# Optimization experiments

Hardware: AMD Instinct MI355X
Metric: run time of the kernel (lower is better)

Reference implementation:

```python
import jax, jax.numpy as jnp
import numpy as np

D, H = 128, 8
N_NODE, N_SRC = 50000, 100000
E_NBR, E_INC = 800000, 200000


def _seg_softmax(scores, idx, n):
    # scores: [E, H]; segmented softmax over segments given by idx
    mx = jax.ops.segment_max(scores, idx, num_segments=n)
    ex = jnp.exp(scores - mx[idx])
    sm = jax.ops.segment_sum(ex, idx, num_segments=n)
    return ex / (sm[idx] + 1e-12)


def _ln(x, g, b):
    m = jnp.mean(x, -1, keepdims=True)
    v = jnp.mean((x - m) ** 2, -1, keepdims=True)
    return g * (x - m) / jnp.sqrt(v + 1e-5) + b


def setup_inputs() -> dict:
    key = jax.random.key(0)
    ks = jax.random.split(key, 24)
    s = 1.0 / np.sqrt(D)
    inp = {
        'X': jax.random.normal(ks[0], (N_NODE, D), jnp.float32),
        'X_src': jax.random.normal(ks[1], (N_SRC, D), jnp.float32),
        'W_qkv': jax.random.normal(ks[2], (D, 3 * D), jnp.float32) * s,
        'w_bias': jax.random.normal(ks[3], (D, H), jnp.float32) * s,
        'W_gate': jax.random.normal(ks[4], (D, D), jnp.float32) * s,
        'b_gate': jnp.zeros((D,), jnp.float32),
        'W_o': jax.random.normal(ks[5], (D, D), jnp.float32) * s,
        'W_q': jax.random.normal(ks[6], (D, D), jnp.float32) * s,
        'W_kv': jax.random.normal(ks[7], (D, 2 * D), jnp.float32) * s,
        'w_bias_tgt': jax.random.normal(ks[8], (D, H), jnp.float32) * s,
        'w_bias_src': jax.random.normal(ks[9], (D, H), jnp.float32) * s,
        'W_gate_tgt': jax.random.normal(ks[10], (D, D), jnp.float32) * s,
        'b_gate_tgt': jnp.zeros((D,), jnp.float32),
        'W_gate_src': jax.random.normal(ks[11], (D, D), jnp.float32) * s,
        'b_gate_src': jnp.zeros((D,), jnp.float32),
        'W_o2': jax.random.normal(ks[12], (D, D), jnp.float32) * s,
        'ln1_g': jnp.ones((D,), jnp.float32),
        'ln1_b': jnp.zeros((D,), jnp.float32),
        'ln2_g': jnp.ones((D,), jnp.float32),
        'ln2_b': jnp.zeros((D,), jnp.float32),
        'nbr_src': jax.random.randint(ks[13], (E_NBR,), 0, N_NODE),
        'nbr_dst': jax.random.randint(ks[14], (E_NBR,), 0, N_NODE),
        'inc_tgt': jax.random.randint(ks[15], (E_INC,), 0, N_NODE),
        'inc_src': jax.random.randint(ks[16], (E_INC,), 0, N_SRC),
    }
    return inp


def reference(X, X_src, W_qkv, w_bias, W_gate, b_gate, W_o, W_q, W_kv,
              w_bias_tgt, w_bias_src, W_gate_tgt, b_gate_tgt, W_gate_src,
              b_gate_src, W_o2, ln1_g, ln1_b, ln2_g, ln2_b,
              nbr_src, nbr_dst, inc_tgt, inc_src):
    N = X.shape[0]
    dk = D // H
    scale = 1.0 / np.sqrt(dk)

    # --- SparseNeighbourhoodSelfAttn on level-0 cells ---
    qkv = (X @ W_qkv).reshape(N, 3, H, dk)
    Q, K, V = qkv[:, 0], qkv[:, 1], qkv[:, 2]            # [N,H,dk]
    scores = jnp.sum(Q[nbr_src] * K[nbr_dst], -1) * scale + (X @ w_bias)[nbr_src]  # [E,H]
    attn = _seg_softmax(scores, nbr_src, N)
    out = jax.ops.segment_sum(attn[..., None] * V[nbr_dst], nbr_src, num_segments=N)  # [N,H,dk]
    gate = jax.nn.sigmoid(X @ W_gate + b_gate).reshape(N, H, dk)
    sa = (gate * out).reshape(N, D) @ W_o
    h = _ln(X + sa, ln1_g, ln1_b)

    # --- SparseTopologicalCrossAttn from level-1 cells ---
    Qc = (h @ W_q).reshape(N, H, dk)
    kv = (X_src @ W_kv).reshape(-1, 2, H, dk)
    Kc, Vc = kv[:, 0], kv[:, 1]
    sc = (jnp.sum(Qc[inc_tgt] * Kc[inc_src], -1) * scale
          + (h @ w_bias_tgt)[inc_tgt] + (X_src @ w_bias_src)[inc_src])  # [Ei,H]
    attn_c = _seg_softmax(sc, inc_tgt, N)
    g_src = jax.nn.sigmoid(X_src @ W_gate_src + b_gate_src).reshape(-1, H, dk)
    out_c = jax.ops.segment_sum(attn_c[..., None] * (g_src[inc_src] * Vc[inc_src]),
                                inc_tgt, num_segments=N)
    g_tgt = jax.nn.sigmoid(h @ W_gate_tgt + b_gate_tgt).reshape(N, H, dk)
    ca = (g_tgt * out_c).reshape(N, D) @ W_o2
    return _ln(h + ca, ln2_g, ln2_b)
```

## Files before the change

### kernel.cpp

```cpp
#include <hip/hip_runtime.h>
#include <stdint.h>

__device__ __forceinline__ float bf_lo(uint32_t w) { return __uint_as_float(w << 16); }
__device__ __forceinline__ float bf_hi(uint32_t w) { return __uint_as_float(w & 0xffff0000u); }
__device__ __forceinline__ float bfu(uint16_t u) { return __uint_as_float((uint32_t)u << 16); }
__device__ __forceinline__ uint16_t f2bf(float f) {
    uint32_t u = __float_as_uint(f);
    uint32_t r = ((u >> 16) & 1u) + 0x7fffu;
    return (uint16_t)((u + r) >> 16);
}
__device__ __forceinline__ uint32_t pk2bf(float a, float b) {
    return (uint32_t)f2bf(a) | ((uint32_t)f2bf(b) << 16);
}
__device__ __forceinline__ void gload_lds16(const void* g, void* l) {
    __builtin_amdgcn_global_load_lds(
        (const __attribute__((address_space(1))) void*)g,
        (__attribute__((address_space(3))) void*)l, 16, 0, 0);
}

typedef __attribute__((ext_vector_type(8))) short bf16x8;
typedef __attribute__((ext_vector_type(4))) float f32x4;

#define LOG2E 1.4426950408889634f
#define QSC2  (0.25f * LOG2E)

#define M_BF16 0
#define M_QS   1
#define M_SIG  2
#define M_KVIK 3
#define M_KVIV 4
#define M_GV   5
#define M_LN1  6
#define M_LN2  7
#define M_B8   8

struct GemmJob {
    const uint16_t* A; const uint16_t* WT; const float* bias;
    const uint16_t* aux; const void* resid;
    const float* lng; const float* lnb;
    void* out; int M; int mode;
};
struct GemmJobs { GemmJob j[6]; };

__global__ __launch_bounds__(256) void multi_gemm_k(GemmJobs jobs)
{
    __shared__ uint16_t As[128 * 128];
    __shared__ uint16_t Ws[128 * 128];
    const GemmJob jb = jobs.j[blockIdx.y];
    const int m0 = blockIdx.x * 128;
    if (m0 >= jb.M) return;
    const int tid = threadIdx.x;
    const int wid = tid >> 6;
    const int lane = tid & 63;
    const int M = jb.M;

    {
        const uint16_t* Ab = jb.A + (size_t)m0 * 128;
        const uint16_t* Wb = jb.WT;
#pragma unroll
        for (int it = 0; it < 8; ++it) {
            int idx = it * 256 + tid;
            int r = idx >> 4, c = idx & 15;
            int gc = c ^ (r & 7);
            uint16_t* ldsA = As + (size_t)(it * 256 + wid * 64) * 8;
            uint16_t* ldsW = Ws + (size_t)(it * 256 + wid * 64) * 8;
            gload_lds16(Ab + (size_t)r * 128 + gc * 8, ldsA);
            gload_lds16(Wb + (size_t)r * 128 + gc * 8, ldsW);
        }
    }
    __syncthreads();

    const int wr = wid >> 1, wc = wid & 1;
    const int l15 = lane & 15, l4 = lane >> 4;
    const int mode = jb.mode;

    if (mode == M_B8) {
        f32x4 acc[4];
#pragma unroll
        for (int i = 0; i < 4; i++) acc[i] = (f32x4){0.f, 0.f, 0.f, 0.f};
#pragma unroll
        for (int kk = 0; kk < 4; ++kk) {
            bf16x8 af0;
            {
                int r = l15;
                int cc = (kk * 4 + l4) ^ (r & 7);
                af0 = *(const bf16x8*)(Ws + r * 128 + cc * 8);
            }
#pragma unroll
            for (int mi = 0; mi < 4; ++mi) {
                int r = wr * 64 + mi * 16 + l15;
                int cc = (kk * 4 + l4) ^ (r & 7);
                bf16x8 bf = *(const bf16x8*)(As + r * 128 + cc * 8);
                acc[mi] = __builtin_amdgcn_mfma_f32_16x16x32_bf16(af0, bf, acc[mi], 0, 0, 0);
            }
        }
        if (wc == 0 && l4 < 2) {
#pragma unroll
            for (int mi = 0; mi < 4; ++mi) {
                int gm = m0 + wr * 64 + mi * 16 + l15;
                if (gm < M) {
                    f32x4 v = acc[mi];
                    *(float4*)((float*)jb.out + (size_t)gm * 8 + l4 * 4) =
                        make_float4(v.x, v.y, v.z, v.w);
                }
            }
        }
        return;
    }

    f32x4 acc[4][4];
#pragma unroll
    for (int i = 0; i < 4; i++)
#pragma unroll
        for (int j = 0; j < 4; j++) acc[i][j] = (f32x4){0.f, 0.f, 0.f, 0.f};

#pragma unroll
    for (int kk = 0; kk < 4; ++kk) {
        bf16x8 af[4], bff[4];
#pragma unroll
        for (int ni = 0; ni < 4; ++ni) {
            int r = wc * 64 + ni * 16 + l15;
            int cc = (kk * 4 + l4) ^ (r & 7);
            af[ni] = *(const bf16x8*)(Ws + r * 128 + cc * 8);
        }
#pragma unroll
        for (int mi = 0; mi < 4; ++mi) {
            int r = wr * 64 + mi * 16 + l15;
            int cc = (kk * 4 + l4) ^ (r & 7);
            bff[mi] = *(const bf16x8*)(As + r * 128 + cc * 8);
        }
#pragma unroll
        for (int ni = 0; ni < 4; ++ni)
#pragma unroll
            for (int mi = 0; mi < 4; ++mi)
                acc[ni][mi] = __builtin_amdgcn_mfma_f32_16x16x32_bf16(
                    af[ni], bff[mi], acc[ni][mi], 0, 0, 0);
    }

    if (mode == M_LN1 || mode == M_LN2) {
        __syncthreads();
        float* redS = (float*)Ws;
        float* redQ = redS + 256;
        float ps[4], qs[4];
#pragma unroll
        for (int mi = 0; mi < 4; ++mi) {
            int row = wr * 64 + mi * 16 + l15;
            int gm = m0 + row;
            float sum = 0.f, sq = 0.f;
#pragma unroll
            for (int ni = 0; ni < 4; ++ni) {
                int gn = wc * 64 + ni * 16 + l4 * 4;
                float r0 = 0.f, r1 = 0.f, r2 = 0.f, r3 = 0.f;
                if (gm < M) {
                    if (mode == M_LN1) {
                        float4 rv = *(const float4*)((const float*)jb.resid + (size_t)gm * 128 + gn);
                        r0 = rv.x; r1 = rv.y; r2 = rv.z; r3 = rv.w;
                    } else {
                        ushort4 rv = *(const ushort4*)((const uint16_t*)jb.resid + (size_t)gm * 128 + gn);
                        r0 = bfu(rv.x); r1 = bfu(rv.y); r2 = bfu(rv.z); r3 = bfu(rv.w);
                    }
                }
                f32x4 t = acc[ni][mi];
                t.x += r0; t.y += r1; t.z += r2; t.w += r3;
                acc[ni][mi] = t;
                sum += t.x + t.y + t.z + t.w;
                sq  += t.x * t.x + t.y * t.y + t.z * t.z + t.w * t.w;
            }
            sum += __shfl_xor(sum, 16); sum += __shfl_xor(sum, 32);
            sq  += __shfl_xor(sq, 16);  sq  += __shfl_xor(sq, 32);
            ps[mi] = sum; qs[mi] = sq;
        }
        if (l4 == 0) {
#pragma unroll
            for (int mi = 0; mi < 4; ++mi) {
                int row = wr * 64 + mi * 16 + l15;
                redS[row * 2 + wc] = ps[mi];
                redQ[row * 2 + wc] = qs[mi];
            }
        }
        __syncthreads();
#pragma unroll
        for (int mi = 0; mi < 4; ++mi) {
            int row = wr * 64 + mi * 16 + l15;
            int gm = m0 + row;
            if (gm >= M) continue;
            float S = redS[row * 2] + redS[row * 2 + 1];
            float Q = redQ[row * 2] + redQ[row * 2 + 1];
            float mean = S * (1.f / 128.f);
            float var  = Q * (1.f / 128.f) - mean * mean;
            float rstd = rsqrtf(var + 1e-5f);
#pragma unroll
            for (int ni = 0; ni < 4; ++ni) {
                int gn = wc * 64 + ni * 16 + l4 * 4;
                float4 gg = *(const float4*)(jb.lng + gn);
                float4 bb = *(const float4*)(jb.lnb + gn);
                f32x4 t = acc[ni][mi];
                float o0 = gg.x * (t.x - mean) * rstd + bb.x;
                float o1 = gg.y * (t.y - mean) * rstd + bb.y;
                float o2 = gg.z * (t.z - mean) * rstd + bb.z;
                float o3 = gg.w * (t.w - mean) * rstd + bb.w;
                if (mode == M_LN1) {
                    ushort4 o;
                    o.x = f2bf(o0); o.y = f2bf(o1); o.z = f2bf(o2); o.w = f2bf(o3);
                    *(ushort4*)((uint16_t*)jb.out + (size_t)gm * 128 + gn) = o;
                } else {
                    *(float4*)((float*)jb.out + (size_t)gm * 128 + gn) =
                        make_float4(o0, o1, o2, o3);
                }
            }
        }
        return;
    }

#pragma unroll
    for (int mi = 0; mi < 4; ++mi) {
        int gm = m0 + wr * 64 + mi * 16 + l15;
        if (gm >= M) continue;
#pragma unroll
        for (int ni = 0; ni < 4; ++ni) {
            int gn = wc * 64 + ni * 16 + l4 * 4;
            f32x4 v = acc[ni][mi];
            if (mode == M_SIG || mode == M_GV) {
                float4 bb = *(const float4*)(jb.bias + gn);
                v.x = 1.f / (1.f + __expf(-(v.x + bb.x)));
                v.y = 1.f / (1.f + __expf(-(v.y + bb.y)));
                v.z = 1.f / (1.f + __expf(-(v.z + bb.z)));
                v.w = 1.f / (1.f + __expf(-(v.w + bb.w)));
            }
            if (mode == M_QS) { v.x *= QSC2; v.y *= QSC2; v.z *= QSC2; v.w *= QSC2; }
            if (mode == M_GV) {
                ushort4 vs = *(const ushort4*)(jb.aux + (size_t)gm * 128 + gn);
                v.x *= bfu(vs.x); v.y *= bfu(vs.y); v.z *= bfu(vs.z); v.w *= bfu(vs.w);
            }
            if (mode == M_KVIK || mode == M_KVIV || mode == M_GV) {
                int which = (mode == M_KVIK) ? 0 : 2;
                uint16_t* op = (uint16_t*)jb.out + (size_t)gm * 256 + gn * 2 + which;
                *reinterpret_cast<uint32_t*>(op)     = pk2bf(v.x, v.y);
                *reinterpret_cast<uint32_t*>(op + 4) = pk2bf(v.z, v.w);
            } else {
                ushort4 o;
                o.x = f2bf(v.x); o.y = f2bf(v.y); o.z = f2bf(v.z); o.w = f2bf(v.w);
                *reinterpret_cast<ushort4*>((uint16_t*)jb.out + (size_t)gm * 128 + gn) = o;
            }
        }
    }
}

#define NBKT_MAX 256
#define CAPSHIFT 14
#define BCAP (1 << CAPSHIFT)

__global__ void castbf2_k(const float* __restrict__ in1, uint16_t* __restrict__ out1, int n1,
                          const float* __restrict__ in2, uint16_t* __restrict__ out2, int n2,
                          int* __restrict__ bktcur)
{
    if (blockIdx.x == 0 && threadIdx.x < NBKT_MAX)
        bktcur[threadIdx.x] = threadIdx.x << CAPSHIFT;
    int i = blockIdx.x * blockDim.x + threadIdx.x;
    int stride = gridDim.x * blockDim.x;
    for (; i < n1 + n2; i += stride) {
        float4 v;
        ushort4 o;
        if (i < n1) v = reinterpret_cast<const float4*>(in1)[i];
        else        v = reinterpret_cast<const float4*>(in2)[i - n1];
        o.x = f2bf(v.x); o.y = f2bf(v.y); o.z = f2bf(v.z); o.w = f2bf(v.w);
        if (i < n1) reinterpret_cast<ushort4*>(out1)[i] = o;
        else        reinterpret_cast<ushort4*>(out2)[i - n1] = o;
    }
}

struct WT14 { const float* src[14]; uint16_t* dst[14]; int nc[14]; int coff[14]; };
__global__ void castWT14_k(WT14 jb)
{
    int y = blockIdx.y;
    const float* W = jb.src[y];
    uint16_t* WT = jb.dst[y];
    int nc = jb.nc[y], coff = jb.coff[y];
    int i = blockIdx.x * 256 + threadIdx.x;
    int k = i >> 7, n = i & 127;
    float v;
    if (nc == 8) v = (n < 8) ? W[k * 8 + n] * LOG2E : 0.f;
    else         v = W[(size_t)k * nc + coff + n];
    WT[(size_t)n * 128 + k] = f2bf(v);
}

__global__ __launch_bounds__(256) void binA_k(
    const int* __restrict__ s1, const int* __restrict__ p1,
    const int* __restrict__ s2, const int* __restrict__ p2,
    int* __restrict__ bktcur, uint2* __restrict__ tmp,
    int E1, int E2, int N, int shift, int nbkt, int chunk)
{
    __shared__ int hist[NBKT_MAX];
    __shared__ int lcur[NBKT_MAX];
    int t = threadIdx.x;
    int Et = E1 + E2;
    int base = blockIdx.x * chunk;
    int end = min(base + chunk, Et);
    for (int i = t; i < nbkt; i += 256) hist[i] = 0;
    __syncthreads();
    for (int i = base + t; i < end; i += 256) {
        int seg = (i < E1) ? s1[i] : N + s2[i - E1];
        atomicAdd(&hist[seg >> shift], 1);
    }
    __syncthreads();
    for (int i = t; i < nbkt; i += 256) {
        int c = hist[i];
        lcur[i] = c ? atomicAdd(&bktcur[i], c) : 0;
    }
    __syncthreads();
    for (int i = base + t; i < end; i += 256) {
        int seg, pay;
        if (i < E1) { seg = s1[i]; pay = p1[i]; }
        else        { seg = N + s2[i - E1]; pay = p2[i - E1]; }
        int p = atomicAdd(&lcur[seg >> shift], 1);
        tmp[p] = make_uint2((uint32_t)seg, (uint32_t)pay);
    }
}

__global__ __launch_bounds__(256) void binD_k(
    const uint2* __restrict__ tmp, const int* __restrict__ bktcur,
    int* __restrict__ offs, int* __restrict__ ends,
    int* __restrict__ sorted, int NN, int spb)
{
    extern __shared__ int sh[];
    __shared__ int wt[4];
    int b = blockIdx.x, t = threadIdx.x;
    int s0 = b * spb;
    int segs = min(spb, NN - s0);
    int p0 = b << CAPSHIFT;
    int p1 = bktcur[b];
    for (int i = t; i < segs; i += 256) sh[i] = 0;
    __syncthreads();
    for (int i = p0 + t; i < p1; i += 256)
        atomicAdd(&sh[(int)tmp[i].x - s0], 1);
    __syncthreads();
    int e_per = (spb + 255) >> 8;
    int loc[4], cv[4]; int ls = 0;
#pragma unroll 4
    for (int j = 0; j < 4; ++j) {
        if (j < e_per) {
            int idx = t * e_per + j;
            int v = (idx < segs) ? sh[idx] : 0;
            loc[j] = ls; cv[j] = v; ls += v;
        }
    }
    int lane = t & 63, w = t >> 6;
    int sc = ls;
#pragma unroll
    for (int o = 1; o < 64; o <<= 1) { int x = __shfl_up(sc, o); if (lane >= o) sc += x; }
    if (lane == 63) wt[w] = sc;
    __syncthreads();
    int add = 0;
    for (int i = 0; i < w; i++) add += wt[i];
    int texcl = add + sc - ls;
#pragma unroll 4
    for (int j = 0; j < 4; ++j) {
        if (j < e_per) {
            int idx = t * e_per + j;
            if (idx < segs) {
                int pos = p0 + texcl + loc[j];
                offs[s0 + idx] = pos;
                ends[s0 + idx] = pos + cv[j];
                sh[idx] = pos;
            }
        }
    }
    __syncthreads();
    for (int i = p0 + t; i < p1; i += 256) {
        uint2 pr = tmp[i];
        int p = atomicAdd(&sh[(int)pr.x - s0], 1);
        sorted[p] = (int)pr.y;
    }
}

#define SEDGE(J, IDX)                                                            \
    {                                                                            \
        int dst = sdst[IDX];                                                     \
        uint2 kv = *reinterpret_cast<const uint2*>(kb + ((size_t)dst << 8));     \
        float s = q0 * bf_lo(kv.x) + q1 * bf_hi(kv.x);                           \
        s += __shfl_xor(s, 1); s += __shfl_xor(s, 2); s += __shfl_xor(s, 4);     \
        float w = exp2f(s + bs);                                                 \
        pa##J = fmaf(w, bf_lo(kv.y), pa##J);                                     \
        pb##J = fmaf(w, bf_hi(kv.y), pb##J);                                     \
        dn##J += w;                                                              \
    }

__global__ __launch_bounds__(256) void self_attn_k(
    const uint16_t* __restrict__ Qb, const uint16_t* __restrict__ kvi,
    const float* __restrict__ bias1,
    const int* __restrict__ offs, const int* __restrict__ ends,
    const int* __restrict__ sdst,
    const uint16_t* __restrict__ g16, uint16_t* __restrict__ Aout, int N)
{
    int lane = threadIdx.x & 63;
    int n = blockIdx.x * 4 + (threadIdx.x >> 6);
    if (n >= N) return;
    uint32_t qw = *reinterpret_cast<const uint32_t*>(Qb + (size_t)n * 128 + 2 * lane);
    float q0 = bf_lo(qw), q1 = bf_hi(qw);
    float bs = bias1[(size_t)n * 8 + (lane >> 3)];
    int e0 = offs[n], e1 = ends[n];
    const uint16_t* kb = kvi + lane * 4;
    float dn0 = 0.f, pa0 = 0.f, pb0 = 0.f;
    float dn1 = 0.f, pa1 = 0.f, pb1 = 0.f;
    int e = e0;
    for (; e + 4 <= e1; e += 4) {
        SEDGE(0, e)
        SEDGE(1, e + 1)
        SEDGE(0, e + 2)
        SEDGE(1, e + 3)
    }
    for (; e < e1; ++e) SEDGE(0, e)
    float den = dn0 + dn1, a0 = pa0 + pa1, a1 = pb0 + pb1;
    float inv = 1.f / (den + 1e-30f);
    uint32_t gw = *reinterpret_cast<const uint32_t*>(g16 + (size_t)n * 128 + 2 * lane);
    a0 *= inv * bf_lo(gw); a1 *= inv * bf_hi(gw);
    *reinterpret_cast<uint32_t*>(Aout + (size_t)n * 128 + 2 * lane) = pk2bf(a0, a1);
}

#define CEDGE(J, IDX)                                                            \
    {                                                                            \
        int src = ssrc[IDX];                                                     \
        uint2 kv = *reinterpret_cast<const uint2*>(kb + ((size_t)src << 8));     \
        float bss = bias_s[(size_t)src * 8 + (lane >> 3)];                       \
        float s = q0 * bf_lo(kv.x) + q1 * bf_hi(kv.x);                           \
        s += __shfl_xor(s, 1); s += __shfl_xor(s, 2); s += __shfl_xor(s, 4);     \
        float w = exp2f(s + bt + bss);                                           \
        pa##J = fmaf(w, bf_lo(kv.y), pa##J);                                     \
        pb##J = fmaf(w, bf_hi(kv.y), pb##J);                                     \
        dn##J += w;                                                              \
    }

__global__ __launch_bounds__(256) void cross_attn_k(
    const uint16_t* __restrict__ Qcb, const float* __restrict__ bias_t,
    const uint16_t* __restrict__ kvgi, const float* __restrict__ bias_s,
    const int* __restrict__ offs, const int* __restrict__ ends,
    const int* __restrict__ ssrc,
    const uint16_t* __restrict__ g16, uint16_t* __restrict__ Aout, int N)
{
    int lane = threadIdx.x & 63;
    int n = blockIdx.x * 4 + (threadIdx.x >> 6);
    if (n >= N) return;
    uint32_t qw = *reinterpret_cast<const uint32_t*>(Qcb + (size_t)n * 128 + 2 * lane);
    float q0 = bf_lo(qw), q1 = bf_hi(qw);
    float bt = bias_t[(size_t)n * 8 + (lane >> 3)];
    int e0 = offs[n], e1 = ends[n];
    const uint16_t* kb = kvgi + lane * 4;
    float dn0 = 0.f, pa0 = 0.f, pb0 = 0.f;
    float dn1 = 0.f, pa1 = 0.f, pb1 = 0.f;
    int e = e0;
    for (; e + 4 <= e1; e += 4) {
        CEDGE(0, e)
        CEDGE(1, e + 1)
        CEDGE(0, e + 2)
        CEDGE(1, e + 3)
    }
    for (; e < e1; ++e) CEDGE(0, e)
    float den = dn0 + dn1, a0 = pa0 + pa1, a1 = pb0 + pb1;
    float inv = 1.f / (den + 1e-30f);
    uint32_t gw = *reinterpret_cast<const uint32_t*>(g16 + (size_t)n * 128 + 2 * lane);
    a0 *= inv * bf_lo(gw); a1 *= inv * bf_hi(gw);
    *reinterpret_cast<uint32_t*>(Aout + (size_t)n * 128 + 2 * lane) = pk2bf(a0, a1);
}

static inline size_t smax_(size_t a, size_t b) { return a > b ? a : b; }

extern "C" void kernel_launch(void* const* d_in, const int* in_sizes, int n_in,
                              void* d_out, int out_size, void* d_ws, size_t ws_size,
                              hipStream_t stream)
{
    const float* X          = (const float*)d_in[0];
    const float* Xs         = (const float*)d_in[1];
    const float* W_qkv      = (const float*)d_in[2];
    const float* w_bias     = (const float*)d_in[3];
    const float* W_gate     = (const float*)d_in[4];
    const float* b_gate     = (const float*)d_in[5];
    const float* W_o        = (const float*)d_in[6];
    const float* W_q        = (const float*)d_in[7];
    const float* W_kv       = (const float*)d_in[8];
    const float* w_bias_tgt = (const float*)d_in[9];
    const float* w_bias_src = (const float*)d_in[10];
    const float* W_gate_tgt = (const float*)d_in[11];
    const float* b_gate_tgt = (const float*)d_in[12];
    const float* W_gate_src = (const float*)d_in[13];
    const float* b_gate_src = (const float*)d_in[14];
    const float* W_o2       = (const float*)d_in[15];
    const float* ln1_g      = (const float*)d_in[16];
    const float* ln1_b      = (const float*)d_in[17];
    const float* ln2_g      = (const float*)d_in[18];
    const float* ln2_b      = (const float*)d_in[19];
    const int* nbr_src      = (const int*)d_in[20];
    const int* nbr_dst      = (const int*)d_in[21];
    const int* inc_tgt      = (const int*)d_in[22];
    const int* inc_src      = (const int*)d_in[23];

    const int N  = in_sizes[0] / 128;
    const int NS = in_sizes[1] / 128;
    const int E1 = in_sizes[20];
    const int E2 = in_sizes[22];
    const int Et = E1 + E2;
    const int NN = 2 * N;
    const int Npad  = (N + 127) & ~127;
    const int NSpad = (NS + 127) & ~127;

    int shift = 9;
    while (((NN + (1 << shift) - 1) >> shift) > NBKT_MAX) ++shift;
    const int spb  = 1 << shift;
    const int nbkt = (NN + spb - 1) >> shift;

    char* ws = (char*)d_ws;
    size_t off = 0;
    auto alloc = [&](size_t bytes) -> void* {
        void* p = ws + off;
        off = (off + bytes + 255) & ~(size_t)255;
        return p;
    };

    uint16_t* Xb   = (uint16_t*)alloc((size_t)Npad * 128 * 2);
    uint16_t* Xsb  = (uint16_t*)alloc((size_t)NSpad * 128 * 2);
    uint16_t* WTq  = (uint16_t*)alloc((size_t)384 * 128 * 2);
    uint16_t* WTkv = (uint16_t*)alloc((size_t)256 * 128 * 2);
    uint16_t* WTg  = (uint16_t*)alloc((size_t)128 * 128 * 2);
    uint16_t* WTo  = (uint16_t*)alloc((size_t)128 * 128 * 2);
    uint16_t* WTq2 = (uint16_t*)alloc((size_t)128 * 128 * 2);
    uint16_t* WTgt = (uint16_t*)alloc((size_t)128 * 128 * 2);
    uint16_t* WTgs = (uint16_t*)alloc((size_t)128 * 128 * 2);
    uint16_t* WTo2 = (uint16_t*)alloc((size_t)128 * 128 * 2);
    uint16_t* WTb1 = (uint16_t*)alloc((size_t)128 * 128 * 2);
    uint16_t* WTbt = (uint16_t*)alloc((size_t)128 * 128 * 2);
    uint16_t* WTbs = (uint16_t*)alloc((size_t)128 * 128 * 2);
    size_t s1a = (size_t)Npad * 384 * 2;
    size_t s1b = (size_t)NSpad * 384 * 2;
    size_t s1c = ((size_t)NBKT_MAX << CAPSHIFT) * 8;
    uint16_t* S1 = (uint16_t*)alloc(smax_(smax_(s1a, s1b), s1c));
    uint16_t* Qb   = S1;
    uint16_t* kvi  = S1 + (size_t)Npad * 128;
    uint16_t* kvgi = S1;
    uint16_t* V16  = S1 + (size_t)NSpad * 256;
    uint2*    tmp  = (uint2*)S1;
    uint16_t* g16  = (uint16_t*)alloc((size_t)N * 128 * 2);
    uint16_t* Qcb  = (uint16_t*)alloc((size_t)N * 128 * 2);
    uint16_t* Awo  = (uint16_t*)alloc((size_t)Npad * 128 * 2);
    uint16_t* hb   = (uint16_t*)alloc((size_t)Npad * 128 * 2);
    float*    b8a  = (float*)alloc((size_t)N * 8 * 4);
    float*    b8s  = (float*)alloc((size_t)NS * 8 * 4);
    int* offs   = (int*)alloc((size_t)NN * 4);
    int* ends   = (int*)alloc((size_t)NN * 4);
    int* sorted = (int*)alloc(((size_t)NBKT_MAX << CAPSHIFT) * 4);
    int* bktcur = (int*)alloc((size_t)NBKT_MAX * 4);
    (void)ws_size; (void)n_in; (void)out_size;

    const int gA  = Npad / 128;
    const int gAs = NSpad / 128;
    const int gW  = (N + 3) / 4;
    const int BINB = 128;
    const int chunk = (Et + BINB - 1) / BINB;

    castbf2_k<<<2048, 256, 0, stream>>>(X, Xb, N * 32, Xs, Xsb, NS * 32, bktcur);
    {
        WT14 jb;
        jb.src[0] = W_qkv; jb.dst[0] = WTq;          jb.nc[0] = 384; jb.coff[0] = 0;
        jb.src[1] = W_qkv; jb.dst[1] = WTq + 16384;  jb.nc[1] = 384; jb.coff[1] = 128;
        jb.src[2] = W_qkv; jb.dst[2] = WTq + 32768;  jb.nc[2] = 384; jb.coff[2] = 256;
        jb.src[3] = W_kv;  jb.dst[3] = WTkv;         jb.nc[3] = 256; jb.coff[3] = 0;
        jb.src[4] = W_kv;  jb.dst[4] = WTkv + 16384; jb.nc[4] = 256; jb.coff[4] = 128;
        jb.src[5] = W_gate;     jb.dst[5] = WTg;  jb.nc[5] = 128; jb.coff[5] = 0;
        jb.src[6] = W_o;        jb.dst[6] = WTo;  jb.nc[6] = 128; jb.coff[6] = 0;
        jb.src[7] = W_q;        jb.dst[7] = WTq2; jb.nc[7] = 128; jb.coff[7] = 0;
        jb.src[8] = W_gate_tgt; jb.dst[8] = WTgt; jb.nc[8] = 128; jb.coff[8] = 0;
        jb.src[9] = W_gate_src; jb.dst[9] = WTgs; jb.nc[9] = 128; jb.coff[9] = 0;
        jb.src[10]= W_o2;       jb.dst[10]= WTo2; jb.nc[10]= 128; jb.coff[10]= 0;
        jb.src[11]= w_bias;     jb.dst[11]= WTb1; jb.nc[11]= 8;   jb.coff[11]= 0;
        jb.src[12]= w_bias_tgt; jb.dst[12]= WTbt; jb.nc[12]= 8;   jb.coff[12]= 0;
        jb.src[13]= w_bias_src; jb.dst[13]= WTbs; jb.nc[13]= 8;   jb.coff[13]= 0;
        castWT14_k<<<dim3(64, 14), 256, 0, stream>>>(jb);
    }

    binA_k<<<BINB, 256, 0, stream>>>(nbr_src, nbr_dst, inc_tgt, inc_src,
                                     bktcur, tmp, E1, E2, N, shift, nbkt, chunk);
    binD_k<<<nbkt, 256, spb * 4, stream>>>(tmp, bktcur, offs, ends, sorted, NN, spb);

    {
        GemmJobs jb{};
        jb.j[0] = { Xb, WTq,         nullptr, nullptr, nullptr, nullptr, nullptr, Qb,  N, M_QS };
        jb.j[1] = { Xb, WTq + 16384, nullptr, nullptr, nullptr, nullptr, nullptr, kvi, N, M_KVIK };
        jb.j[2] = { Xb, WTq + 32768, nullptr, nullptr, nullptr, nullptr, nullptr, kvi, N, M_KVIV };
        jb.j[3] = { Xb, WTg,         b_gate,  nullptr, nullptr, nullptr, nullptr, g16, N, M_SIG };
        jb.j[4] = { Xb, WTb1,        nullptr, nullptr, nullptr, nullptr, nullptr, b8a, N, M_B8 };
        multi_gemm_k<<<dim3(gA, 5), 256, 0, stream>>>(jb);
    }
    self_attn_k<<<gW, 256, 0, stream>>>(Qb, kvi, b8a, offs, ends, sorted, g16, Awo, N);
    {
        GemmJobs jb{};
        jb.j[0] = { Awo, WTo, nullptr, nullptr, X, ln1_g, ln1_b, hb, N, M_LN1 };
        multi_gemm_k<<<dim3(gA, 1), 256, 0, stream>>>(jb);
    }
    {
        GemmJobs jb{};
        jb.j[0] = { hb,  WTq2,         nullptr,    nullptr, nullptr, nullptr, nullptr, Qcb,  N,  M_QS };
        jb.j[1] = { hb,  WTgt,         b_gate_tgt, nullptr, nullptr, nullptr, nullptr, g16,  N,  M_SIG };
        jb.j[2] = { Xsb, WTkv,         nullptr,    nullptr, nullptr, nullptr, nullptr, kvgi, NS, M_KVIK };
        jb.j[3] = { Xsb, WTkv + 16384, nullptr,    nullptr, nullptr, nullptr, nullptr, V16,  NS, M_BF16 };
        jb.j[4] = { hb,  WTbt,         nullptr,    nullptr, nullptr, nullptr, nullptr, b8a,  N,  M_B8 };
        multi_gemm_k<<<dim3(gAs, 5), 256, 0, stream>>>(jb);
    }
    {
        GemmJobs jb{};
        jb.j[0] = { Xsb, WTgs, b_gate_src, V16, nullptr, nullptr, nullptr, kvgi, NS, M_GV };
        jb.j[1] = { Xsb, WTbs, nullptr, nullptr, nullptr, nullptr, nullptr, b8s,  NS, M_B8 };
        multi_gemm_k<<<dim3(gAs, 2), 256, 0, stream>>>(jb);
    }
    cross_attn_k<<<gW, 256, 0, stream>>>(Qcb, b8a, kvgi, b8s, offs + N, ends + N, sorted, g16, Awo, N);
    {
        GemmJobs jb{};
        jb.j[0] = { Awo, WTo2, nullptr, nullptr, hb, ln2_g, ln2_b, d_out, N, M_LN2 };
        multi_gemm_k<<<dim3(gA, 1), 256, 0, stream>>>(jb);
    }
}
```

Measured before the change: 328.6 us.

## Fuse prep kernels, merge gated-V GEMM, scalarize edge indices in attention

Merges the input cast, weight transpose and bucket-histogram kernels into one prep launch, with a memset replacing the cursor initialisation. Computes the source gate and V projection inside one GEMM block (M_GV2), which removes the separate V16 round trip and one launch. Rewrites both attention kernels to load edge indices as wave-uniform scalars, issue four independent gathers per iteration, and use 128-thread blocks. These changes reduce launch count and global traffic, at the cost of a heavier GEMM job with two sequential MFMA passes and more register pressure.

```diff
diff --git a/kernel.cpp b/kernel.cpp
--- a/kernel.cpp
+++ b/kernel.cpp
@@ -29,10 +29,10 @@
 #define M_SIG  2
 #define M_KVIK 3
 #define M_KVIV 4
-#define M_GV   5
 #define M_LN1  6
 #define M_LN2  7
 #define M_B8   8
+#define M_GV2  9
 
 struct GemmJob {
     const uint16_t* A; const uint16_t* WT; const float* bias;
@@ -41,6 +41,19 @@
     void* out; int M; int mode;
 };
 struct GemmJobs { GemmJob j[6]; };
+
+__device__ __forceinline__ void stage_tile(const uint16_t* __restrict__ g,
+                                           uint16_t* lds, int tid, int wid)
+{
+#pragma unroll
+    for (int it = 0; it < 8; ++it) {
+        int idx = it * 256 + tid;
+        int r = idx >> 4, c = idx & 15;
+        int gc = c ^ (r & 7);
+        gload_lds16(g + (size_t)r * 128 + gc * 8,
+                    lds + (size_t)(it * 256 + wid * 64) * 8);
+    }
+}
 
 __global__ __launch_bounds__(256) void multi_gemm_k(GemmJobs jobs)
 {
@@ -54,20 +67,8 @@
     const int lane = tid & 63;
     const int M = jb.M;
 
-    {
-        const uint16_t* Ab = jb.A + (size_t)m0 * 128;
-        const uint16_t* Wb = jb.WT;
-#pragma unroll
-        for (int it = 0; it < 8; ++it) {
-            int idx = it * 256 + tid;
-            int r = idx >> 4, c = idx & 15;
-            int gc = c ^ (r & 7);
-            uint16_t* ldsA = As + (size_t)(it * 256 + wid * 64) * 8;
-            uint16_t* ldsW = Ws + (size_t)(it * 256 + wid * 64) * 8;
-            gload_lds16(Ab + (size_t)r * 128 + gc * 8, ldsA);
-            gload_lds16(Wb + (size_t)r * 128 + gc * 8, ldsW);
-        }
-    }
+    stage_tile(jb.A + (size_t)m0 * 128, As, tid, wid);
+    stage_tile(jb.WT, Ws, tid, wid);
     __syncthreads();
 
     const int wr = wid >> 1, wc = wid & 1;
@@ -103,6 +104,95 @@
                     *(float4*)((float*)jb.out + (size_t)gm * 8 + l4 * 4) =
                         make_float4(v.x, v.y, v.z, v.w);
                 }
+            }
+        }
+        return;
+    }
+
+    if (mode == M_GV2) {
+        f32x4 acc[4][4];
+#pragma unroll
+        for (int i = 0; i < 4; i++)
+#pragma unroll
+            for (int j = 0; j < 4; j++) acc[i][j] = (f32x4){0.f, 0.f, 0.f, 0.f};
+#pragma unroll
+        for (int kk = 0; kk < 4; ++kk) {
+            bf16x8 af[4], bff[4];
+#pragma unroll
+            for (int ni = 0; ni < 4; ++ni) {
+                int r = wc * 64 + ni * 16 + l15;
+                int cc = (kk * 4 + l4) ^ (r & 7);
+                af[ni] = *(const bf16x8*)(Ws + r * 128 + cc * 8);
+            }
+#pragma unroll
+            for (int mi = 0; mi < 4; ++mi) {
+                int r = wr * 64 + mi * 16 + l15;
+                int cc = (kk * 4 + l4) ^ (r & 7);
+                bff[mi] = *(const bf16x8*)(As + r * 128 + cc * 8);
+            }
+#pragma unroll
+            for (int ni = 0; ni < 4; ++ni)
+#pragma unroll
+                for (int mi = 0; mi < 4; ++mi)
+                    acc[ni][mi] = __builtin_amdgcn_mfma_f32_16x16x32_bf16(
+                        af[ni], bff[mi], acc[ni][mi], 0, 0, 0);
+        }
+        uint32_t gpk[4][4][2];
+#pragma unroll
+        for (int ni = 0; ni < 4; ++ni) {
+            int gn = wc * 64 + ni * 16 + l4 * 4;
+            float4 bb = *(const float4*)(jb.bias + gn);
+#pragma unroll
+            for (int mi = 0; mi < 4; ++mi) {
+                f32x4 v = acc[ni][mi];
+                float g0 = 1.f / (1.f + __expf(-(v.x + bb.x)));
+                float g1 = 1.f / (1.f + __expf(-(v.y + bb.y)));
+                float g2 = 1.f / (1.f + __expf(-(v.z + bb.z)));
+                float g3 = 1.f / (1.f + __expf(-(v.w + bb.w)));
+                gpk[ni][mi][0] = pk2bf(g0, g1);
+                gpk[ni][mi][1] = pk2bf(g2, g3);
+                acc[ni][mi] = (f32x4){0.f, 0.f, 0.f, 0.f};
+            }
+        }
+        __syncthreads();
+        stage_tile(jb.aux, Ws, tid, wid);
+        __syncthreads();
+#pragma unroll
+        for (int kk = 0; kk < 4; ++kk) {
+            bf16x8 af[4], bff[4];
+#pragma unroll
+            for (int ni = 0; ni < 4; ++ni) {
+                int r = wc * 64 + ni * 16 + l15;
+                int cc = (kk * 4 + l4) ^ (r & 7);
+                af[ni] = *(const bf16x8*)(Ws + r * 128 + cc * 8);
+            }
+#pragma unroll
+            for (int mi = 0; mi < 4; ++mi) {
+                int r = wr * 64 + mi * 16 + l15;
+                int cc = (kk * 4 + l4) ^ (r & 7);
+                bff[mi] = *(const bf16x8*)(As + r * 128 + cc * 8);
+            }
+#pragma unroll
+            for (int ni = 0; ni < 4; ++ni)
+#pragma unroll
+                for (int mi = 0; mi < 4; ++mi)
+                    acc[ni][mi] = __builtin_amdgcn_mfma_f32_16x16x32_bf16(
+                        af[ni], bff[mi], acc[ni][mi], 0, 0, 0);
+        }
+#pragma unroll
+        for (int mi = 0; mi < 4; ++mi) {
+            int gm = m0 + wr * 64 + mi * 16 + l15;
+            if (gm >= M) continue;
+#pragma unroll
+            for (int ni = 0; ni < 4; ++ni) {
+                int gn = wc * 64 + ni * 16 + l4 * 4;
+                f32x4 v = acc[ni][mi];
+                uint32_t g01 = gpk[ni][mi][0], g23 = gpk[ni][mi][1];
+                v.x *= bf_lo(g01); v.y *= bf_hi(g01);
+                v.z *= bf_lo(g23); v.w *= bf_hi(g23);
+                uint16_t* op = (uint16_t*)jb.out + (size_t)gm * 256 + gn * 2 + 2;
+                *reinterpret_cast<uint32_t*>(op)     = pk2bf(v.x, v.y);
+                *reinterpret_cast<uint32_t*>(op + 4) = pk2bf(v.z, v.w);
             }
         }
         return;
@@ -220,7 +310,7 @@
         for (int ni = 0; ni < 4; ++ni) {
             int gn = wc * 64 + ni * 16 + l4 * 4;
             f32x4 v = acc[ni][mi];
-            if (mode == M_SIG || mode == M_GV) {
+            if (mode == M_SIG) {
                 float4 bb = *(const float4*)(jb.bias + gn);
                 v.x = 1.f / (1.f + __expf(-(v.x + bb.x)));
                 v.y = 1.f / (1.f + __expf(-(v.y + bb.y)));
@@ -228,11 +318,7 @@
                 v.w = 1.f / (1.f + __expf(-(v.w + bb.w)));
             }
             if (mode == M_QS) { v.x *= QSC2; v.y *= QSC2; v.z *= QSC2; v.w *= QSC2; }
-            if (mode == M_GV) {
-                ushort4 vs = *(const ushort4*)(jb.aux + (size_t)gm * 128 + gn);
-                v.x *= bfu(vs.x); v.y *= bfu(vs.y); v.z *= bfu(vs.z); v.w *= bfu(vs.w);
-            }
-            if (mode == M_KVIK || mode == M_KVIV || mode == M_GV) {
+            if (mode == M_KVIK || mode == M_KVIV) {
                 int which = (mode == M_KVIK) ? 0 : 2;
                 uint16_t* op = (uint16_t*)jb.out + (size_t)gm * 256 + gn * 2 + which;
                 *reinterpret_cast<uint32_t*>(op)     = pk2bf(v.x, v.y);
@@ -250,75 +336,77 @@
 #define CAPSHIFT 14
 #define BCAP (1 << CAPSHIFT)
 
-__global__ void castbf2_k(const float* __restrict__ in1, uint16_t* __restrict__ out1, int n1,
-                          const float* __restrict__ in2, uint16_t* __restrict__ out2, int n2,
-                          int* __restrict__ bktcur)
-{
-    if (blockIdx.x == 0 && threadIdx.x < NBKT_MAX)
-        bktcur[threadIdx.x] = threadIdx.x << CAPSHIFT;
-    int i = blockIdx.x * blockDim.x + threadIdx.x;
-    int stride = gridDim.x * blockDim.x;
-    for (; i < n1 + n2; i += stride) {
-        float4 v;
-        ushort4 o;
-        if (i < n1) v = reinterpret_cast<const float4*>(in1)[i];
-        else        v = reinterpret_cast<const float4*>(in2)[i - n1];
-        o.x = f2bf(v.x); o.y = f2bf(v.y); o.z = f2bf(v.z); o.w = f2bf(v.w);
-        if (i < n1) reinterpret_cast<ushort4*>(out1)[i] = o;
-        else        reinterpret_cast<ushort4*>(out2)[i - n1] = o;
-    }
-}
+#define PREP_CAST_BLKS 2048
+#define PREP_WT_BLKS   896
 
 struct WT14 { const float* src[14]; uint16_t* dst[14]; int nc[14]; int coff[14]; };
-__global__ void castWT14_k(WT14 jb)
-{
-    int y = blockIdx.y;
-    const float* W = jb.src[y];
-    uint16_t* WT = jb.dst[y];
-    int nc = jb.nc[y], coff = jb.coff[y];
-    int i = blockIdx.x * 256 + threadIdx.x;
-    int k = i >> 7, n = i & 127;
-    float v;
-    if (nc == 8) v = (n < 8) ? W[k * 8 + n] * LOG2E : 0.f;
-    else         v = W[(size_t)k * nc + coff + n];
-    WT[(size_t)n * 128 + k] = f2bf(v);
-}
-
-__global__ __launch_bounds__(256) void binA_k(
+
+__global__ __launch_bounds__(256) void prep_k(
+    const float* __restrict__ X, uint16_t* __restrict__ Xb, int n1,
+    const float* __restrict__ Xs, uint16_t* __restrict__ Xsb, int n2,
+    WT14 wt,
     const int* __restrict__ s1, const int* __restrict__ p1,
     const int* __restrict__ s2, const int* __restrict__ p2,
-    int* __restrict__ bktcur, uint2* __restrict__ tmp,
+    int* __restrict__ bktcnt, uint2* __restrict__ tmp,
     int E1, int E2, int N, int shift, int nbkt, int chunk)
 {
     __shared__ int hist[NBKT_MAX];
     __shared__ int lcur[NBKT_MAX];
+    int bx = blockIdx.x;
     int t = threadIdx.x;
-    int Et = E1 + E2;
-    int base = blockIdx.x * chunk;
-    int end = min(base + chunk, Et);
-    for (int i = t; i < nbkt; i += 256) hist[i] = 0;
-    __syncthreads();
-    for (int i = base + t; i < end; i += 256) {
-        int seg = (i < E1) ? s1[i] : N + s2[i - E1];
-        atomicAdd(&hist[seg >> shift], 1);
-    }
-    __syncthreads();
-    for (int i = t; i < nbkt; i += 256) {
-        int c = hist[i];
-        lcur[i] = c ? atomicAdd(&bktcur[i], c) : 0;
-    }
-    __syncthreads();
-    for (int i = base + t; i < end; i += 256) {
-        int seg, pay;
-        if (i < E1) { seg = s1[i]; pay = p1[i]; }
-        else        { seg = N + s2[i - E1]; pay = p2[i - E1]; }
-        int p = atomicAdd(&lcur[seg >> shift], 1);
-        tmp[p] = make_uint2((uint32_t)seg, (uint32_t)pay);
+    if (bx < PREP_CAST_BLKS) {
+        int i = bx * 256 + t;
+        int stride = PREP_CAST_BLKS * 256;
+        for (; i < n1 + n2; i += stride) {
+            float4 v;
+            ushort4 o;
+            if (i < n1) v = reinterpret_cast<const float4*>(X)[i];
+            else        v = reinterpret_cast<const float4*>(Xs)[i - n1];
+            o.x = f2bf(v.x); o.y = f2bf(v.y); o.z = f2bf(v.z); o.w = f2bf(v.w);
+            if (i < n1) reinterpret_cast<ushort4*>(Xb)[i] = o;
+            else        reinterpret_cast<ushort4*>(Xsb)[i - n1] = o;
+        }
+    } else if (bx < PREP_CAST_BLKS + PREP_WT_BLKS) {
+        int pb = bx - PREP_CAST_BLKS;
+        int y = pb >> 6, xx = pb & 63;
+        const float* W = wt.src[y];
+        uint16_t* WT = wt.dst[y];
+        int nc = wt.nc[y], coff = wt.coff[y];
+        int i = xx * 256 + t;
+        int k = i >> 7, n = i & 127;
+        float v;
+        if (nc == 8) v = (n < 8) ? W[k * 8 + n] * LOG2E : 0.f;
+        else         v = W[(size_t)k * nc + coff + n];
+        WT[(size_t)n * 128 + k] = f2bf(v);
+    } else {
+        int bid = bx - (PREP_CAST_BLKS + PREP_WT_BLKS);
+        int Et = E1 + E2;
+        int base = bid * chunk;
+        int end = min(base + chunk, Et);
+        for (int i = t; i < nbkt; i += 256) hist[i] = 0;
+        __syncthreads();
+        for (int i = base + t; i < end; i += 256) {
+            int seg = (i < E1) ? s1[i] : N + s2[i - E1];
+            atomicAdd(&hist[seg >> shift], 1);
+        }
+        __syncthreads();
+        for (int i = t; i < nbkt; i += 256) {
+            int c = hist[i];
+            lcur[i] = (i << CAPSHIFT) + (c ? atomicAdd(&bktcnt[i], c) : 0);
+        }
+        __syncthreads();
+        for (int i = base + t; i < end; i += 256) {
+            int seg, pay;
+            if (i < E1) { seg = s1[i]; pay = p1[i]; }
+            else        { seg = N + s2[i - E1]; pay = p2[i - E1]; }
+            int p = atomicAdd(&lcur[seg >> shift], 1);
+            tmp[p] = make_uint2((uint32_t)seg, (uint32_t)pay);
+        }
     }
 }
 
 __global__ __launch_bounds__(256) void binD_k(
-    const uint2* __restrict__ tmp, const int* __restrict__ bktcur,
+    const uint2* __restrict__ tmp, const int* __restrict__ bktcnt,
     int* __restrict__ offs, int* __restrict__ ends,
     int* __restrict__ sorted, int NN, int spb)
 {
@@ -328,7 +416,7 @@
     int s0 = b * spb;
     int segs = min(spb, NN - s0);
     int p0 = b << CAPSHIFT;
-    int p1 = bktcur[b];
+    int p1 = p0 + bktcnt[b];
     for (int i = t; i < segs; i += 256) sh[i] = 0;
     __syncthreads();
     for (int i = p0 + t; i < p1; i += 256)
@@ -373,19 +461,17 @@
     }
 }
 
-#define SEDGE(J, IDX)                                                            \
+#define SSTEP(KV, ACC)                                                           \
     {                                                                            \
-        int dst = sdst[IDX];                                                     \
-        uint2 kv = *reinterpret_cast<const uint2*>(kb + ((size_t)dst << 8));     \
-        float s = q0 * bf_lo(kv.x) + q1 * bf_hi(kv.x);                           \
+        float s = q0 * bf_lo(KV.x) + q1 * bf_hi(KV.x);                           \
         s += __shfl_xor(s, 1); s += __shfl_xor(s, 2); s += __shfl_xor(s, 4);     \
         float w = exp2f(s + bs);                                                 \
-        pa##J = fmaf(w, bf_lo(kv.y), pa##J);                                     \
-        pb##J = fmaf(w, bf_hi(kv.y), pb##J);                                     \
-        dn##J += w;                                                              \
-    }
-
-__global__ __launch_bounds__(256) void self_attn_k(
+        pa##ACC = fmaf(w, bf_lo(KV.y), pa##ACC);                                 \
+        pb##ACC = fmaf(w, bf_hi(KV.y), pb##ACC);                                 \
+        dn##ACC += w;                                                            \
+    }
+
+__global__ __launch_bounds__(128) void self_attn_k(
     const uint16_t* __restrict__ Qb, const uint16_t* __restrict__ kvi,
     const float* __restrict__ bias1,
     const int* __restrict__ offs, const int* __restrict__ ends,
@@ -393,44 +479,55 @@
     const uint16_t* __restrict__ g16, uint16_t* __restrict__ Aout, int N)
 {
     int lane = threadIdx.x & 63;
-    int n = blockIdx.x * 4 + (threadIdx.x >> 6);
+    int n = blockIdx.x * 2 + (threadIdx.x >> 6);
     if (n >= N) return;
+    const int lane4 = lane * 4;
     uint32_t qw = *reinterpret_cast<const uint32_t*>(Qb + (size_t)n * 128 + 2 * lane);
     float q0 = bf_lo(qw), q1 = bf_hi(qw);
     float bs = bias1[(size_t)n * 8 + (lane >> 3)];
     int e0 = offs[n], e1 = ends[n];
-    const uint16_t* kb = kvi + lane * 4;
     float dn0 = 0.f, pa0 = 0.f, pb0 = 0.f;
     float dn1 = 0.f, pa1 = 0.f, pb1 = 0.f;
+    float dn2 = 0.f, pa2 = 0.f, pb2 = 0.f;
+    float dn3 = 0.f, pa3 = 0.f, pb3 = 0.f;
     int e = e0;
     for (; e + 4 <= e1; e += 4) {
-        SEDGE(0, e)
-        SEDGE(1, e + 1)
-        SEDGE(0, e + 2)
-        SEDGE(1, e + 3)
-    }
-    for (; e < e1; ++e) SEDGE(0, e)
-    float den = dn0 + dn1, a0 = pa0 + pa1, a1 = pb0 + pb1;
+        const int* sp = sdst + __builtin_amdgcn_readfirstlane(e);
+        int d0 = __builtin_amdgcn_readfirstlane(sp[0]);
+        int d1 = __builtin_amdgcn_readfirstlane(sp[1]);
+        int d2 = __builtin_amdgcn_readfirstlane(sp[2]);
+        int d3 = __builtin_amdgcn_readfirstlane(sp[3]);
+        uint2 kv0 = *reinterpret_cast<const uint2*>(kvi + ((size_t)d0 << 8) + lane4);
+        uint2 kv1 = *reinterpret_cast<const uint2*>(kvi + ((size_t)d1 << 8) + lane4);
+        uint2 kv2 = *reinterpret_cast<const uint2*>(kvi + ((size_t)d2 << 8) + lane4);
+        uint2 kv3 = *reinterpret_cast<const uint2*>(kvi + ((size_t)d3 << 8) + lane4);
+        SSTEP(kv0, 0) SSTEP(kv1, 1) SSTEP(kv2, 2) SSTEP(kv3, 3)
+    }
+    for (; e < e1; ++e) {
+        int d0 = __builtin_amdgcn_readfirstlane(sdst[__builtin_amdgcn_readfirstlane(e)]);
+        uint2 kv0 = *reinterpret_cast<const uint2*>(kvi + ((size_t)d0 << 8) + lane4);
+        SSTEP(kv0, 0)
+    }
+    float den = (dn0 + dn1) + (dn2 + dn3);
+    float a0 = (pa0 + pa1) + (pa2 + pa3);
+    float a1 = (pb0 + pb1) + (pb2 + pb3);
     float inv = 1.f / (den + 1e-30f);
     uint32_t gw = *reinterpret_cast<const uint32_t*>(g16 + (size_t)n * 128 + 2 * lane);
     a0 *= inv * bf_lo(gw); a1 *= inv * bf_hi(gw);
     *reinterpret_cast<uint32_t*>(Aout + (size_t)n * 128 + 2 * lane) = pk2bf(a0, a1);
 }
 
-#define CEDGE(J, IDX)                                                            \
+#define CSTEP(KV, BSS, ACC)                                                      \
     {                                                                            \
-        int src = ssrc[IDX];                                                     \
-        uint2 kv = *reinterpret_cast<const uint2*>(kb + ((size_t)src << 8));     \
-        float bss = bias_s[(size_t)src * 8 + (lane >> 3)];                       \
-        float s = q0 * bf_lo(kv.x) + q1 * bf_hi(kv.x);                           \
+        float s = q0 * bf_lo(KV.x) + q1 * bf_hi(KV.x);                           \
         s += __shfl_xor(s, 1); s += __shfl_xor(s, 2); s += __shfl_xor(s, 4);     \
-        float w = exp2f(s + bt + bss);                                           \
-        pa##J = fmaf(w, bf_lo(kv.y), pa##J);                                     \
-        pb##J = fmaf(w, bf_hi(kv.y), pb##J);                                     \
-        dn##J += w;                                                              \
-    }
-
-__global__ __launch_bounds__(256) void cross_attn_k(
+        float w = exp2f(s + bt + BSS);                                           \
+        pa##ACC = fmaf(w, bf_lo(KV.y), pa##ACC);                                 \
+        pb##ACC = fmaf(w, bf_hi(KV.y), pb##ACC);                                 \
+        dn##ACC += w;                                                            \
+    }
+
+__global__ __launch_bounds__(128) void cross_attn_k(
     const uint16_t* __restrict__ Qcb, const float* __restrict__ bias_t,
     const uint16_t* __restrict__ kvgi, const float* __restrict__ bias_s,
     const int* __restrict__ offs, const int* __restrict__ ends,
@@ -438,24 +535,44 @@
     const uint16_t* __restrict__ g16, uint16_t* __restrict__ Aout, int N)
 {
     int lane = threadIdx.x & 63;
-    int n = blockIdx.x * 4 + (threadIdx.x >> 6);
+    int n = blockIdx.x * 2 + (threadIdx.x >> 6);
     if (n >= N) return;
+    const int lane4 = lane * 4;
+    const int head = lane >> 3;
     uint32_t qw = *reinterpret_cast<const uint32_t*>(Qcb + (size_t)n * 128 + 2 * lane);
     float q0 = bf_lo(qw), q1 = bf_hi(qw);
-    float bt = bias_t[(size_t)n * 8 + (lane >> 3)];
+    float bt = bias_t[(size_t)n * 8 + head];
     int e0 = offs[n], e1 = ends[n];
-    const uint16_t* kb = kvgi + lane * 4;
     float dn0 = 0.f, pa0 = 0.f, pb0 = 0.f;
     float dn1 = 0.f, pa1 = 0.f, pb1 = 0.f;
+    float dn2 = 0.f, pa2 = 0.f, pb2 = 0.f;
+    float dn3 = 0.f, pa3 = 0.f, pb3 = 0.f;
     int e = e0;
     for (; e + 4 <= e1; e += 4) {
-        CEDGE(0, e)
-        CEDGE(1, e + 1)
-        CEDGE(0, e + 2)
-        CEDGE(1, e + 3)
-    }
-    for (; e < e1; ++e) CEDGE(0, e)
-    float den = dn0 + dn1, a0 = pa0 + pa1, a1 = pb0 + pb1;
+        const int* sp = ssrc + __builtin_amdgcn_readfirstlane(e);
+        int d0 = __builtin_amdgcn_readfirstlane(sp[0]);
+        int d1 = __builtin_amdgcn_readfirstlane(sp[1]);
+        int d2 = __builtin_amdgcn_readfirstlane(sp[2]);
+        int d3 = __builtin_amdgcn_readfirstlane(sp[3]);
+        uint2 kv0 = *reinterpret_cast<const uint2*>(kvgi + ((size_t)d0 << 8) + lane4);
+        uint2 kv1 = *reinterpret_cast<const uint2*>(kvgi + ((size_t)d1 << 8) + lane4);
+        uint2 kv2 = *reinterpret_cast<const uint2*>(kvgi + ((size_t)d2 << 8) + lane4);
+        uint2 kv3 = *reinterpret_cast<const uint2*>(kvgi + ((size_t)d3 << 8) + lane4);
+        float bs0 = (bias_s + (size_t)d0 * 8)[head];
+        float bs1 = (bias_s + (size_t)d1 * 8)[head];
+        float bs2 = (bias_s + (size_t)d2 * 8)[head];
+        float bs3 = (bias_s + (size_t)d3 * 8)[head];
+        CSTEP(kv0, bs0, 0) CSTEP(kv1, bs1, 1) CSTEP(kv2, bs2, 2) CSTEP(kv3, bs3, 3)
+    }
+    for (; e < e1; ++e) {
+        int d0 = __builtin_amdgcn_readfirstlane(ssrc[__builtin_amdgcn_readfirstlane(e)]);
+        uint2 kv0 = *reinterpret_cast<const uint2*>(kvgi + ((size_t)d0 << 8) + lane4);
+        float bs0 = (bias_s + (size_t)d0 * 8)[head];
+        CSTEP(kv0, bs0, 0)
+    }
+    float den = (dn0 + dn1) + (dn2 + dn3);
+    float a0 = (pa0 + pa1) + (pa2 + pa3);
+    float a1 = (pb0 + pb1) + (pb2 + pb3);
     float inv = 1.f / (den + 1e-30f);
     uint32_t gw = *reinterpret_cast<const uint32_t*>(g16 + (size_t)n * 128 + 2 * lane);
     a0 *= inv * bf_lo(gw); a1 *= inv * bf_hi(gw);
@@ -535,7 +652,6 @@
     uint16_t* Qb   = S1;
     uint16_t* kvi  = S1 + (size_t)Npad * 128;
     uint16_t* kvgi = S1;
-    uint16_t* V16  = S1 + (size_t)NSpad * 256;
     uint2*    tmp  = (uint2*)S1;
     uint16_t* g16  = (uint16_t*)alloc((size_t)N * 128 * 2);
     uint16_t* Qcb  = (uint16_t*)alloc((size_t)N * 128 * 2);
@@ -546,38 +662,38 @@
     int* offs   = (int*)alloc((size_t)NN * 4);
     int* ends   = (int*)alloc((size_t)NN * 4);
     int* sorted = (int*)alloc(((size_t)NBKT_MAX << CAPSHIFT) * 4);
-    int* bktcur = (int*)alloc((size_t)NBKT_MAX * 4);
+    int* bktcnt = (int*)alloc((size_t)NBKT_MAX * 4);
     (void)ws_size; (void)n_in; (void)out_size;
 
     const int gA  = Npad / 128;
     const int gAs = NSpad / 128;
-    const int gW  = (N + 3) / 4;
+    const int gW  = (N + 1) / 2;
     const int BINB = 128;
     const int chunk = (Et + BINB - 1) / BINB;
 
-    castbf2_k<<<2048, 256, 0, stream>>>(X, Xb, N * 32, Xs, Xsb, NS * 32, bktcur);
+    hipMemsetAsync(bktcnt, 0, (size_t)NBKT_MAX * 4, stream);
     {
-        WT14 jb;
-        jb.src[0] = W_qkv; jb.dst[0] = WTq;          jb.nc[0] = 384; jb.coff[0] = 0;
-        jb.src[1] = W_qkv; jb.dst[1] = WTq + 16384;  jb.nc[1] = 384; jb.coff[1] = 128;
-        jb.src[2] = W_qkv; jb.dst[2] = WTq + 32768;  jb.nc[2] = 384; jb.coff[2] = 256;
-        jb.src[3] = W_kv;  jb.dst[3] = WTkv;         jb.nc[3] = 256; jb.coff[3] = 0;
-        jb.src[4] = W_kv;  jb.dst[4] = WTkv + 16384; jb.nc[4] = 256; jb.coff[4] = 128;
-        jb.src[5] = W_gate;     jb.dst[5] = WTg;  jb.nc[5] = 128; jb.coff[5] = 0;
-        jb.src[6] = W_o;        jb.dst[6] = WTo;  jb.nc[6] = 128; jb.coff[6] = 0;
-        jb.src[7] = W_q;        jb.dst[7] = WTq2; jb.nc[7] = 128; jb.coff[7] = 0;
-        jb.src[8] = W_gate_tgt; jb.dst[8] = WTgt; jb.nc[8] = 128; jb.coff[8] = 0;
-        jb.src[9] = W_gate_src; jb.dst[9] = WTgs; jb.nc[9] = 128; jb.coff[9] = 0;
-        jb.src[10]= W_o2;       jb.dst[10]= WTo2; jb.nc[10]= 128; jb.coff[10]= 0;
-        jb.src[11]= w_bias;     jb.dst[11]= WTb1; jb.nc[11]= 8;   jb.coff[11]= 0;
-        jb.src[12]= w_bias_tgt; jb.dst[12]= WTbt; jb.nc[12]= 8;   jb.coff[12]= 0;
-        jb.src[13]= w_bias_src; jb.dst[13]= WTbs; jb.nc[13]= 8;   jb.coff[13]= 0;
-        castWT14_k<<<dim3(64, 14), 256, 0, stream>>>(jb);
-    }
-
-    binA_k<<<BINB, 256, 0, stream>>>(nbr_src, nbr_dst, inc_tgt, inc_src,
-                                     bktcur, tmp, E1, E2, N, shift, nbkt, chunk);
-    binD_k<<<nbkt, 256, spb * 4, stream>>>(tmp, bktcur, offs, ends, sorted, NN, spb);
+        WT14 wt;
+        wt.src[0] = W_qkv; wt.dst[0] = WTq;          wt.nc[0] = 384; wt.coff[0] = 0;
+        wt.src[1] = W_qkv; wt.dst[1] = WTq + 16384;  wt.nc[1] = 384; wt.coff[1] = 128;
+        wt.src[2] = W_qkv; wt.dst[2] = WTq + 32768;  wt.nc[2] = 384; wt.coff[2] = 256;
+        wt.src[3] = W_kv;  wt.dst[3] = WTkv;         wt.nc[3] = 256; wt.coff[3] = 0;
+        wt.src[4] = W_kv;  wt.dst[4] = WTkv + 16384; wt.nc[4] = 256; wt.coff[4] = 128;
+        wt.src[5] = W_gate;     wt.dst[5] = WTg;  wt.nc[5] = 128; wt.coff[5] = 0;
+        wt.src[6] = W_o;        wt.dst[6] = WTo;  wt.nc[6] = 128; wt.coff[6] = 0;
+        wt.src[7] = W_q;        wt.dst[7] = WTq2; wt.nc[7] = 128; wt.coff[7] = 0;
+        wt.src[8] = W_gate_tgt; wt.dst[8] = WTgt; wt.nc[8] = 128; wt.coff[8] = 0;
+        wt.src[9] = W_gate_src; wt.dst[9] = WTgs; wt.nc[9] = 128; wt.coff[9] = 0;
+        wt.src[10]= W_o2;       wt.dst[10]= WTo2; wt.nc[10]= 128; wt.coff[10]= 0;
+        wt.src[11]= w_bias;     wt.dst[11]= WTb1; wt.nc[11]= 8;   wt.coff[11]= 0;
+        wt.src[12]= w_bias_tgt; wt.dst[12]= WTbt; wt.nc[12]= 8;   wt.coff[12]= 0;
+        wt.src[13]= w_bias_src; wt.dst[13]= WTbs; wt.nc[13]= 8;   wt.coff[13]= 0;
+        prep_k<<<PREP_CAST_BLKS + PREP_WT_BLKS + BINB, 256, 0, stream>>>(
+            X, Xb, N * 32, Xs, Xsb, NS * 32, wt,
+            nbr_src, nbr_dst, inc_tgt, inc_src,
+            bktcnt, tmp, E1, E2, N, shift, nbkt, chunk);
+    }
+    binD_k<<<nbkt, 256, spb * 4, stream>>>(tmp, bktcnt, offs, ends, sorted, NN, spb);
 
     {
         GemmJobs jb{};
@@ -588,7 +704,7 @@
         jb.j[4] = { Xb, WTb1,        nullptr, nullptr, nullptr, nullptr, nullptr, b8a, N, M_B8 };
         multi_gemm_k<<<dim3(gA, 5), 256, 0, stream>>>(jb);
     }
-    self_attn_k<<<gW, 256, 0, stream>>>(Qb, kvi, b8a, offs, ends, sorted, g16, Awo, N);
+    self_attn_k<<<gW, 128, 0, stream>>>(Qb, kvi, b8a, offs, ends, sorted, g16, Awo, N);
     {
         GemmJobs jb{};
         jb.j[0] = { Awo, WTo, nullptr, nullptr, X, ln1_g, ln1_b, hb, N, M_LN1 };
@@ -596,20 +712,15 @@
     }
     {
         GemmJobs jb{};
-        jb.j[0] = { hb,  WTq2,         nullptr,    nullptr, nullptr, nullptr, nullptr, Qcb,  N,  M_QS };
-        jb.j[1] = { hb,  WTgt,         b_gate_tgt, nullptr, nullptr, nullptr, nullptr, g16,  N,  M_SIG };
-        jb.j[2] = { Xsb, WTkv,         nullptr,    nullptr, nullptr, nullptr, nullptr, kvgi, NS, M_KVIK };
-        jb.j[3] = { Xsb, WTkv + 16384, nullptr,    nullptr, nullptr, nullptr, nullptr, V16,  NS, M_BF16 };
-        jb.j[4] = { hb,  WTbt,         nullptr,    nullptr, nullptr, nullptr, nullptr, b8a,  N,  M_B8 };
-        multi_gemm_k<<<dim3(gAs, 5), 256, 0, stream>>>(jb);
-    }
-    {
-        GemmJobs jb{};
-        jb.j[0] = { Xsb, WTgs, b_gate_src, V16, nullptr, nullptr, nullptr, kvgi, NS, M_GV };
-        jb.j[1] = { Xsb, WTbs, nullptr, nullptr, nullptr, nullptr, nullptr, b8s,  NS, M_B8 };
-        multi_gemm_k<<<dim3(gAs, 2), 256, 0, stream>>>(jb);
-    }
-    cross_attn_k<<<gW, 256, 0, stream>>>(Qcb, b8a, kvgi, b8s, offs + N, ends + N, sorted, g16, Awo, N);
+        jb.j[0] = { hb,  WTq2,         nullptr,    nullptr,       nullptr, nullptr, nullptr, Qcb,  N,  M_QS };
+        jb.j[1] = { hb,  WTgt,         b_gate_tgt, nullptr,       nullptr, nullptr, nullptr, g16,  N,  M_SIG };
+        jb.j[2] = { Xsb, WTkv,         nullptr,    nullptr,       nullptr, nullptr, nullptr, kvgi, NS, M_KVIK };
+        jb.j[3] = { Xsb, WTgs,         b_gate_src, WTkv + 16384,  nullptr, nullptr, nullptr, kvgi, NS, M_GV2 };
+        jb.j[4] = { hb,  WTbt,         nullptr,    nullptr,       nullptr, nullptr, nullptr, b8a,  N,  M_B8 };
+        jb.j[5] = { Xsb, WTbs,         nullptr,    nullptr,       nullptr, nullptr, nullptr, b8s,  NS, M_B8 };
+        multi_gemm_k<<<dim3(gAs, 6), 256, 0, stream>>>(jb);
+    }
+    cross_attn_k<<<gW, 128, 0, stream>>>(Qcb, b8a, kvgi, b8s, offs + N, ends + N, sorted, g16, Awo, N);
     {
         GemmJobs jb{};
         jb.j[0] = { Awo, WTo2, nullptr, nullptr, hb, ln2_g, ln2_b, d_out, N, M_LN2 };
```

Result: no change. 333.6 us (+1.5%).
